# Kernel optimization log

Measured on AMD Instinct MI355X. Metric: run time of the kernel, lower is better.

## Reference

```python
import jax, jax.numpy as jnp
import numpy as np

EPS = 1e-5
K = 3
N_TAP = K * K


def _bn(x, g, b, m, v):
    # eval-mode batchnorm over channel axis 1 of NCHW
    inv = g / jnp.sqrt(v + EPS)
    return x * inv[None, :, None, None] + (b - m * inv)[None, :, None, None]


def _silu(x):
    return x * jax.nn.sigmoid(x)


def _dcn(x, offset, mask, w, b, pad=1):
    """Modulated deformable conv (DCNv2), stride 1.
    x: [B,C,H,W], offset: [B,2n,H,W] ((dy,dx) per tap), mask: [B,n,H,W],
    w: [O,C,K,K], b: [O]."""
    B, C, H, W = x.shape
    O = w.shape[0]
    ky, kx = jnp.meshgrid(jnp.arange(K), jnp.arange(K), indexing='ij')
    ky = ky.reshape(N_TAP).astype(x.dtype)
    kx = kx.reshape(N_TAP).astype(x.dtype)
    off = offset.reshape(B, N_TAP, 2, H, W)
    base_y = jnp.arange(H, dtype=x.dtype)[None, None, :, None]
    base_x = jnp.arange(W, dtype=x.dtype)[None, None, None, :]
    # fractional sample positions [B,n,H,W]
    py = base_y - pad + ky[None, :, None, None] + off[:, :, 0]
    px = base_x - pad + kx[None, :, None, None] + off[:, :, 1]
    y0 = jnp.floor(py)
    x0 = jnp.floor(px)
    fy = py - y0
    fx = px - x0
    y0i = y0.astype(jnp.int32)
    x0i = x0.astype(jnp.int32)
    x_flat = x.reshape(B, C, 1, H * W)

    def corner(yi, xi, wgt):
        valid = (yi >= 0) & (yi < H) & (xi >= 0) & (xi < W)
        idx = (jnp.clip(yi, 0, H - 1) * W + jnp.clip(xi, 0, W - 1)).reshape(B, 1, N_TAP, H * W)
        v = jnp.take_along_axis(x_flat, idx, axis=-1)  # [B,C,n,HW]
        return v * (wgt * valid.astype(x.dtype)).reshape(B, 1, N_TAP, H * W)

    acc = corner(y0i, x0i, (1 - fy) * (1 - fx))
    acc = acc + corner(y0i, x0i + 1, (1 - fy) * fx)
    acc = acc + corner(y0i + 1, x0i, fy * (1 - fx))
    acc = acc + corner(y0i + 1, x0i + 1, fy * fx)
    val = acc.reshape(B, C, N_TAP, H, W) * mask[:, None]  # modulation
    out = jnp.einsum('bcnhw,ocn->bohw', val, w.reshape(O, C, N_TAP))
    return out + b[None, :, None, None]


def setup_inputs() -> dict:
    key = jax.random.key(0)
    ks = jax.random.split(key, 16)
    B, C1, H, W = 8, 256, 80, 80
    C2 = 256
    Ch = 128  # c_ = int(c2 * 0.5)
    d = {}
    d['x'] = jax.random.normal(ks[0], (B, C1, H, W), jnp.float32)
    # cv1: 1x1 conv (no bias) + BN
    d['cv1_w'] = jax.random.normal(ks[1], (Ch, C1), jnp.float32) * (1.0 / np.sqrt(C1))
    d['bn1_g'] = jax.random.uniform(ks[2], (Ch,), jnp.float32, 0.5, 1.5)
    d['bn1_b'] = jax.random.normal(ks[3], (Ch,), jnp.float32) * 0.1
    d['bn1_m'] = jax.random.normal(ks[4], (Ch,), jnp.float32) * 0.1
    d['bn1_v'] = jax.random.uniform(ks[5], (Ch,), jnp.float32, 0.5, 1.5)
    # offset/mask predictor 3x3 conv (small weights -> modest deformation)
    d['off_w'] = jax.random.normal(ks[6], (3 * N_TAP, Ch, K, K), jnp.float32) * 0.01
    d['off_b'] = jnp.zeros((3 * N_TAP,), jnp.float32)
    # dcn main weight/bias
    d['dcn_w'] = jax.random.normal(ks[7], (Ch, Ch, K, K), jnp.float32) * (1.0 / np.sqrt(Ch * N_TAP))
    d['dcn_b'] = jnp.zeros((Ch,), jnp.float32)
    d['bn2_g'] = jax.random.uniform(ks[8], (Ch,), jnp.float32, 0.5, 1.5)
    d['bn2_b'] = jax.random.normal(ks[9], (Ch,), jnp.float32) * 0.1
    d['bn2_m'] = jax.random.normal(ks[10], (Ch,), jnp.float32) * 0.1
    d['bn2_v'] = jax.random.uniform(ks[11], (Ch,), jnp.float32, 0.5, 1.5)
    # cv2: 1x1 conv (no bias) + BN
    d['cv2_w'] = jax.random.normal(ks[12], (C2, Ch), jnp.float32) * (1.0 / np.sqrt(Ch))
    d['bn3_g'] = jax.random.uniform(ks[13], (C2,), jnp.float32, 0.5, 1.5)
    d['bn3_b'] = jax.random.normal(ks[14], (C2,), jnp.float32) * 0.1
    d['bn3_m'] = jax.random.normal(ks[15], (C2,), jnp.float32) * 0.1
    d['bn3_v'] = jnp.ones((C2,), jnp.float32)
    return d


def reference(x, cv1_w, bn1_g, bn1_b, bn1_m, bn1_v,
              off_w, off_b, dcn_w, dcn_b, bn2_g, bn2_b, bn2_m, bn2_v,
              cv2_w, bn3_g, bn3_b, bn3_m, bn3_v):
    # cv1: 1x1 conv -> BN -> SiLU
    y = _silu(_bn(jnp.einsum('bchw,oc->bohw', x, cv1_w), bn1_g, bn1_b, bn1_m, bn1_v))
    # offset/mask predictor: 3x3 conv, pad 1
    raw = jax.lax.conv_general_dilated(
        y, off_w, window_strides=(1, 1), padding=((1, 1), (1, 1)),
        dimension_numbers=('NCHW', 'OIHW', 'NCHW')) + off_b[None, :, None, None]
    offset = raw[:, :2 * N_TAP]
    mask = jax.nn.sigmoid(raw[:, 2 * N_TAP:])
    # modulated deformable 3x3 conv -> BN -> SiLU
    y = _silu(_bn(_dcn(y, offset, mask, dcn_w, dcn_b), bn2_g, bn2_b, bn2_m, bn2_v))
    # cv2: 1x1 conv -> BN -> SiLU
    y = _silu(_bn(jnp.einsum('bchw,oc->bohw', y, cv2_w), bn3_g, bn3_b, bn3_m, bn3_v))
    return x + y  # shortcut (c1 == c2)
```

## Files before the change

### kernel.cpp

```cpp
#include <hip/hip_runtime.h>
#include <math.h>

#define HWSZ 6400
#define WIMG 80
#define HIMG 80
#define BEPS 1e-5f

typedef __attribute__((ext_vector_type(8))) short short8;
typedef __attribute__((ext_vector_type(4))) float f32x4;

__device__ __forceinline__ unsigned short f2b(float f) {
    unsigned u = __builtin_bit_cast(unsigned, f);
    u += 0x7fffu + ((u >> 16) & 1u);
    return (unsigned short)(u >> 16);
}
__device__ __forceinline__ float b2f(unsigned short h) {
    unsigned u = ((unsigned)h) << 16;
    return __builtin_bit_cast(float, u);
}
__device__ __forceinline__ float silu_f(float t) { return t / (1.f + __expf(-t)); }

#define BPOS(sub, nt, n16, q) (((((sub)*4 + (nt))*16 + (n16))*40) + (q)*8)

__global__ __launch_bounds__(256) void k_prep(
    const float* __restrict__ cv1w, const float* __restrict__ g1, const float* __restrict__ b1,
    const float* __restrict__ m1, const float* __restrict__ v1,
    const float* __restrict__ offw, const float* __restrict__ offb,
    const float* __restrict__ dcnw, const float* __restrict__ dcnb,
    const float* __restrict__ g2, const float* __restrict__ b2,
    const float* __restrict__ m2, const float* __restrict__ v2,
    const float* __restrict__ cv2w, const float* __restrict__ g3, const float* __restrict__ b3,
    const float* __restrict__ m3, const float* __restrict__ v3,
    unsigned short* __restrict__ apk1, unsigned short* __restrict__ apko,
    unsigned short* __restrict__ apkd, unsigned short* __restrict__ apk2,
    float* __restrict__ bias1, float* __restrict__ biaso,
    float* __restrict__ bias2, float* __restrict__ bias3)
{
    int idx = blockIdx.x * 256 + threadIdx.x;
    if (idx < 32768) {
        int j = idx & 7, L = (idx >> 3) & 63, ks = (idx >> 9) & 7, mt = idx >> 12;
        int o = mt * 16 + (L & 15), k = ks * 32 + (L >> 4) * 8 + j;
        float inv = g1[o] * rsqrtf(v1[o] + BEPS);
        apk1[idx] = f2b(cv1w[o * 256 + k] * inv);
    } else if (idx < 69632) {
        int t = idx - 32768;
        int j = t & 7, L = (t >> 3) & 63;
        int mt = t / 18432, rem = t % 18432, ks = rem >> 9;
        int o = mt * 16 + (L & 15);
        int kp = ks * 32 + (L >> 4) * 8 + j;
        int n = kp >> 7, c = kp & 127;
        float wv = (o < 27) ? offw[(size_t)(o * 128 + c) * 9 + n] : 0.f;
        apko[t] = f2b(wv);
    } else if (idx < 217088) {
        int t = idx - 69632;
        int j = t & 7, L = (t >> 3) & 63;
        int mt = t / 18432, rem = t % 18432, ks = rem >> 9;
        int o = mt * 16 + (L & 15);
        int kp = ks * 32 + (L >> 4) * 8 + j;
        int n = kp >> 7, c = kp & 127;
        float inv = g2[o] * rsqrtf(v2[o] + BEPS);
        apkd[t] = f2b(dcnw[(size_t)(o * 128 + c) * 9 + n] * inv);
    } else if (idx < 249856) {
        int t = idx - 217088;
        int j = t & 7, L = (t >> 3) & 63, ks = (t >> 9) & 3, mt = t >> 11;
        int o = mt * 16 + (L & 15), k = ks * 32 + (L >> 4) * 8 + j;
        float inv = g3[o] * rsqrtf(v3[o] + BEPS);
        apk2[t] = f2b(cv2w[o * 128 + k] * inv);
    } else if (idx < 250395) {
        int t = idx - 249856;
        if (t < 128) { float inv = g1[t] * rsqrtf(v1[t] + BEPS); bias1[t] = b1[t] - m1[t] * inv; }
        else if (t < 155) { biaso[t - 128] = offb[t - 128]; }
        else if (t < 283) { int o = t - 155; float inv = g2[o] * rsqrtf(v2[o] + BEPS);
                            bias2[o] = dcnb[o] * inv + b2[o] - m2[o] * inv; }
        else { int o = t - 283; float inv = g3[o] * rsqrtf(v3[o] + BEPS); bias3[o] = b3[o] - m3[o] * inv; }
    }
}

__global__ __launch_bounds__(256) void k_cv1(
    const float* __restrict__ x, const unsigned short* __restrict__ apk1,
    const float* __restrict__ bias1, unsigned short* __restrict__ y1t)
{
    __shared__ __align__(16) unsigned short sB[20480];
    int blk = blockIdx.x;
    int b = blk / 100, pt = blk % 100;
    int p0 = pt * 64;
    int tid = threadIdx.x;
    int lane = tid & 63;
    int w = tid >> 6;
    {
        int px = lane, q = w;
        const float* xb = x + (size_t)b * 256 * HWSZ + p0 + px;
        for (int ks = 0; ks < 8; ++ks) {
            short8 v;
#pragma unroll
            for (int j = 0; j < 8; ++j)
                v[j] = (short)f2b(xb[(size_t)(ks * 32 + q * 8 + j) * HWSZ]);
            *(short8*)&sB[((ks * 4 + (px >> 4)) * 16 + (px & 15)) * 40 + q * 8] = v;
        }
    }
    __syncthreads();
    int n16 = lane & 15, qd = lane >> 4;
    f32x4 acc[2][4];
#pragma unroll
    for (int mi = 0; mi < 2; ++mi)
#pragma unroll
        for (int nt = 0; nt < 4; ++nt) acc[mi][nt] = (f32x4){0.f, 0.f, 0.f, 0.f};
    for (int ks = 0; ks < 8; ++ks) {
        short8 bf[4];
#pragma unroll
        for (int nt = 0; nt < 4; ++nt)
            bf[nt] = *(const short8*)&sB[((ks * 4 + nt) * 16 + n16) * 40 + qd * 8];
#pragma unroll
        for (int mi = 0; mi < 2; ++mi) {
            int mt = w * 2 + mi;
            short8 af = *(const short8*)&apk1[(size_t)((mt * 8 + ks) * 64 + lane) * 8];
#pragma unroll
            for (int nt = 0; nt < 4; ++nt)
                acc[mi][nt] = __builtin_amdgcn_mfma_f32_16x16x32_bf16(af, bf[nt], acc[mi][nt], 0, 0, 0);
        }
    }
    __syncthreads();
#pragma unroll
    for (int mi = 0; mi < 2; ++mi)
#pragma unroll
        for (int nt = 0; nt < 4; ++nt)
#pragma unroll
            for (int r = 0; r < 4; ++r) {
                int o = w * 32 + mi * 16 + qd * 4 + r;
                float sv = silu_f(acc[mi][nt][r] + bias1[o]);
                sB[(nt * 16 + n16) * 136 + o] = f2b(sv);
            }
    __syncthreads();
    {
        int px = tid >> 2, qq = tid & 3;
        unsigned short* ytb = y1t + ((size_t)b * HWSZ + p0 + px) * 128;
#pragma unroll
        for (int seg = 0; seg < 4; ++seg) {
            short8 v = *(const short8*)&sB[px * 136 + qq * 32 + seg * 8];
            *(short8*)&ytb[qq * 32 + seg * 8] = v;
        }
    }
}

__global__ __launch_bounds__(256) void k_off(
    const unsigned short* __restrict__ y1t, const unsigned short* __restrict__ apko,
    const float* __restrict__ biaso, float* __restrict__ raw)
{
    __shared__ __align__(16) unsigned short sV[10240];
    int blk = blockIdx.x;
    int b = blk / 100, pt = blk % 100;
    int p0 = pt * 64;
    int tid = threadIdx.x;
    int lane = tid & 63, w = tid >> 6;
    int n16 = lane & 15, qd = lane >> 4;
    int pxl = tid >> 2, q = tid & 3;
    int p = p0 + pxl;
    int h = p / WIMG, wx = p % WIMG;
    const unsigned short* yb = y1t + (size_t)b * HWSZ * 128;
    f32x4 acc[2];
    acc[0] = (f32x4){0.f, 0.f, 0.f, 0.f};
    acc[1] = (f32x4){0.f, 0.f, 0.f, 0.f};
    const short8 zz = {0, 0, 0, 0, 0, 0, 0, 0};
    for (int n = 0; n < 9; ++n) {
        int hh = h - 1 + n / 3, ww = wx - 1 + n % 3;
        bool valid = ((unsigned)hh < HIMG) && ((unsigned)ww < WIMG);
        int spx = valid ? hh * WIMG + ww : 0;
        const unsigned short* ys = yb + (size_t)spx * 128 + q * 8;
#pragma unroll
        for (int sub = 0; sub < 4; ++sub) {
            short8 v = *(const short8*)&ys[sub * 32];
            if (!valid) v = zz;
            *(short8*)&sV[BPOS(sub, pxl >> 4, pxl & 15, q)] = v;
        }
        __syncthreads();
#pragma unroll
        for (int sub = 0; sub < 4; ++sub) {
            int ks = n * 4 + sub;
            short8 bf = *(const short8*)&sV[BPOS(sub, w, n16, qd)];
#pragma unroll
            for (int mi = 0; mi < 2; ++mi) {
                short8 af = *(const short8*)&apko[(size_t)((mi * 36 + ks) * 64 + lane) * 8];
                acc[mi] = __builtin_amdgcn_mfma_f32_16x16x32_bf16(af, bf, acc[mi], 0, 0, 0);
            }
        }
        __syncthreads();
    }
    float* rb = raw + (size_t)b * 27 * HWSZ + p0 + w * 16 + n16;
#pragma unroll
    for (int mi = 0; mi < 2; ++mi)
#pragma unroll
        for (int r = 0; r < 4; ++r) {
            int o = mi * 16 + qd * 4 + r;
            if (o < 27) {
                float t = acc[mi][r] + biaso[o];
                if (o >= 18) t = 1.f / (1.f + __expf(-t));
                rb[(size_t)o * HWSZ] = t;
            }
        }
}

__global__ __launch_bounds__(256) void k_dcn(
    const unsigned short* __restrict__ y1t, const float* __restrict__ raw,
    const unsigned short* __restrict__ apkd, const float* __restrict__ bias2,
    unsigned short* __restrict__ zt)
{
    __shared__ float swgt[4][9][64];
    __shared__ unsigned short sidx[4][9][64];
    __shared__ __align__(16) unsigned short sV[10240];
    int blk = blockIdx.x;
    int b = blk / 100, pt = blk % 100;
    int p0 = pt * 64;
    int tid = threadIdx.x;

    for (int i = tid; i < 576; i += 256) {
        int n = i / 64, pp = i % 64;
        int p = p0 + pp;
        int h = p / WIMG, wx = p % WIMG;
        const float* rb = raw + (size_t)b * 27 * HWSZ + p;
        float dy = rb[(size_t)(2 * n) * HWSZ];
        float dx = rb[(size_t)(2 * n + 1) * HWSZ];
        float mk = rb[(size_t)(18 + n) * HWSZ];
        float py = (float)(h - 1 + n / 3) + dy;
        float px = (float)(wx - 1 + n % 3) + dx;
        float y0f = floorf(py), x0f = floorf(px);
        float fy = py - y0f, fx = px - x0f;
        int y0 = (int)y0f, x0 = (int)x0f;
#pragma unroll
        for (int k = 0; k < 4; ++k) {
            int yy = y0 + (k >> 1);
            int xx = x0 + (k & 1);
            bool valid = ((unsigned)yy < HIMG) && ((unsigned)xx < WIMG);
            float wk = ((k >> 1) ? fy : 1.f - fy) * ((k & 1) ? fx : 1.f - fx);
            wk = valid ? wk * mk : 0.f;
            int yc = min(max(yy, 0), HIMG - 1);
            int xc = min(max(xx, 0), WIMG - 1);
            sidx[k][n][pp] = (unsigned short)(yc * WIMG + xc);
            swgt[k][n][pp] = wk;
        }
    }
    __syncthreads();

    int lane = tid & 63, w = tid >> 6;
    int n16 = lane & 15, qd = lane >> 4;
    int pxl = tid >> 2, q = tid & 3;
    const unsigned short* yb = y1t + (size_t)b * HWSZ * 128;
    f32x4 acc[2][4];
#pragma unroll
    for (int mi = 0; mi < 2; ++mi)
#pragma unroll
        for (int nt = 0; nt < 4; ++nt) acc[mi][nt] = (f32x4){0.f, 0.f, 0.f, 0.f};

    for (int n = 0; n < 9; ++n) {
        float av[4][8];
#pragma unroll
        for (int sub = 0; sub < 4; ++sub)
#pragma unroll
            for (int j = 0; j < 8; ++j) av[sub][j] = 0.f;
#pragma unroll
        for (int k = 0; k < 4; ++k) {
            float wk = swgt[k][n][pxl];
            const unsigned short* ys = yb + (size_t)sidx[k][n][pxl] * 128 + q * 8;
#pragma unroll
            for (int sub = 0; sub < 4; ++sub) {
                short8 v = *(const short8*)&ys[sub * 32];
#pragma unroll
                for (int j = 0; j < 8; ++j)
                    av[sub][j] = fmaf(wk, b2f((unsigned short)v[j]), av[sub][j]);
            }
        }
#pragma unroll
        for (int sub = 0; sub < 4; ++sub) {
            short8 v;
#pragma unroll
            for (int j = 0; j < 8; ++j) v[j] = (short)f2b(av[sub][j]);
            *(short8*)&sV[BPOS(sub, pxl >> 4, pxl & 15, q)] = v;
        }
        __syncthreads();
#pragma unroll
        for (int sub = 0; sub < 4; ++sub) {
            int ks = n * 4 + sub;
            short8 bf[4];
#pragma unroll
            for (int nt = 0; nt < 4; ++nt)
                bf[nt] = *(const short8*)&sV[BPOS(sub, nt, n16, qd)];
#pragma unroll
            for (int mi = 0; mi < 2; ++mi) {
                short8 af = *(const short8*)&apkd[(size_t)(((2 * w + mi) * 36 + ks) * 64 + lane) * 8];
#pragma unroll
                for (int nt = 0; nt < 4; ++nt)
                    acc[mi][nt] = __builtin_amdgcn_mfma_f32_16x16x32_bf16(af, bf[nt], acc[mi][nt], 0, 0, 0);
            }
        }
        __syncthreads();
    }
#pragma unroll
    for (int mi = 0; mi < 2; ++mi)
#pragma unroll
        for (int nt = 0; nt < 4; ++nt)
#pragma unroll
            for (int r = 0; r < 4; ++r) {
                int o = w * 32 + mi * 16 + qd * 4 + r;
                float sv = silu_f(acc[mi][nt][r] + bias2[o]);
                sV[(nt * 16 + n16) * 136 + o] = f2b(sv);
            }
    __syncthreads();
    {
        int px = tid >> 2, qq = tid & 3;
        unsigned short* zb = zt + ((size_t)b * HWSZ + p0 + px) * 128;
#pragma unroll
        for (int seg = 0; seg < 4; ++seg) {
            short8 v = *(const short8*)&sV[px * 136 + qq * 32 + seg * 8];
            *(short8*)&zb[qq * 32 + seg * 8] = v;
        }
    }
}

__global__ __launch_bounds__(256) void k_cv2(
    const unsigned short* __restrict__ zt, const float* __restrict__ x,
    const unsigned short* __restrict__ apk2, const float* __restrict__ bias3,
    float* __restrict__ out)
{
    int blk = blockIdx.x;
    int b = blk / 100, pt = blk % 100;
    int p0 = pt * 64;
    int tid = threadIdx.x;
    int lane = tid & 63, w = tid >> 6;
    int n16 = lane & 15, qd = lane >> 4;
    const unsigned short* zb = zt + ((size_t)b * HWSZ + p0) * 128;
    f32x4 acc[4][4];
#pragma unroll
    for (int mi = 0; mi < 4; ++mi)
#pragma unroll
        for (int nt = 0; nt < 4; ++nt) acc[mi][nt] = (f32x4){0.f, 0.f, 0.f, 0.f};
#pragma unroll
    for (int ks = 0; ks < 4; ++ks) {
        short8 bf[4];
#pragma unroll
        for (int nt = 0; nt < 4; ++nt)
            bf[nt] = *(const short8*)&zb[(size_t)(nt * 16 + n16) * 128 + ks * 32 + qd * 8];
#pragma unroll
        for (int mi = 0; mi < 4; ++mi) {
            int mt = w * 4 + mi;
            short8 af = *(const short8*)&apk2[(size_t)((mt * 4 + ks) * 64 + lane) * 8];
#pragma unroll
            for (int nt = 0; nt < 4; ++nt)
                acc[mi][nt] = __builtin_amdgcn_mfma_f32_16x16x32_bf16(af, bf[nt], acc[mi][nt], 0, 0, 0);
        }
    }
    const float* xb = x + (size_t)b * 256 * HWSZ;
    float* ob = out + (size_t)b * 256 * HWSZ;
#pragma unroll
    for (int mi = 0; mi < 4; ++mi)
#pragma unroll
        for (int nt = 0; nt < 4; ++nt)
#pragma unroll
            for (int r = 0; r < 4; ++r) {
                int o = w * 64 + mi * 16 + qd * 4 + r;
                size_t idx = (size_t)o * HWSZ + p0 + nt * 16 + n16;
                ob[idx] = xb[idx] + silu_f(acc[mi][nt][r] + bias3[o]);
            }
}

extern "C" void kernel_launch(void* const* d_in, const int* in_sizes, int n_in,
                              void* d_out, int out_size, void* d_ws, size_t ws_size,
                              hipStream_t stream) {
    const float* x     = (const float*)d_in[0];
    const float* cv1w  = (const float*)d_in[1];
    const float* bn1g  = (const float*)d_in[2];
    const float* bn1b  = (const float*)d_in[3];
    const float* bn1m  = (const float*)d_in[4];
    const float* bn1v  = (const float*)d_in[5];
    const float* offw  = (const float*)d_in[6];
    const float* offb  = (const float*)d_in[7];
    const float* dcnw  = (const float*)d_in[8];
    const float* dcnb  = (const float*)d_in[9];
    const float* bn2g  = (const float*)d_in[10];
    const float* bn2b  = (const float*)d_in[11];
    const float* bn2m  = (const float*)d_in[12];
    const float* bn2v  = (const float*)d_in[13];
    const float* cv2w  = (const float*)d_in[14];
    const float* bn3g  = (const float*)d_in[15];
    const float* bn3b  = (const float*)d_in[16];
    const float* bn3m  = (const float*)d_in[17];
    const float* bn3v  = (const float*)d_in[18];
    float* out = (float*)d_out;

    float* base = (float*)d_ws;
    unsigned short* y1t = (unsigned short*)base;
    float* raw   = base + 3276800;
    unsigned short* zt  = (unsigned short*)(base + 4659200);
    unsigned short* apk1 = (unsigned short*)(base + 7936000);
    unsigned short* apko = (unsigned short*)(base + 7952384);
    unsigned short* apkd = (unsigned short*)(base + 7970816);
    unsigned short* apk2 = (unsigned short*)(base + 8044544);
    float* bias1 = base + 8060928;
    float* biaso = base + 8061056;
    float* bias2 = base + 8061088;
    float* bias3 = base + 8061216;

    k_prep<<<979, 256, 0, stream>>>(cv1w, bn1g, bn1b, bn1m, bn1v,
                                    offw, offb, dcnw, dcnb,
                                    bn2g, bn2b, bn2m, bn2v,
                                    cv2w, bn3g, bn3b, bn3m, bn3v,
                                    apk1, apko, apkd, apk2,
                                    bias1, biaso, bias2, bias3);
    k_cv1<<<800, 256, 0, stream>>>(x, apk1, bias1, y1t);
    k_off<<<800, 256, 0, stream>>>(y1t, apko, biaso, raw);
    k_dcn<<<800, 256, 0, stream>>>(y1t, raw, apkd, bias2, zt);
    k_cv2<<<800, 256, 0, stream>>>(zt, x, apk2, bias3, out);
}
```

Before: 235.9 us.

## Stage halo tiles in LDS for offset conv and deformable sampling, remap blocks

Measured after the change: 262.8 us. 11.4% more time.

```diff
diff --git a/kernel.cpp b/kernel.cpp
--- a/kernel.cpp
+++ b/kernel.cpp
@@ -8,6 +8,7 @@
 
 typedef __attribute__((ext_vector_type(8))) short short8;
 typedef __attribute__((ext_vector_type(4))) float f32x4;
+typedef __attribute__((ext_vector_type(4))) unsigned u32x4;
 
 __device__ __forceinline__ unsigned short f2b(float f) {
     unsigned u = __builtin_bit_cast(unsigned, f);
@@ -20,7 +21,7 @@
 }
 __device__ __forceinline__ float silu_f(float t) { return t / (1.f + __expf(-t)); }
 
-#define BPOS(sub, nt, n16, q) (((((sub)*4 + (nt))*16 + (n16))*40) + (q)*8)
+__device__ __forceinline__ int remap800(int blk) { return (blk & 7) * 100 + (blk >> 3); }
 
 __global__ __launch_bounds__(256) void k_prep(
     const float* __restrict__ cv1w, const float* __restrict__ g1, const float* __restrict__ b1,
@@ -81,7 +82,7 @@
     const float* __restrict__ bias1, unsigned short* __restrict__ y1t)
 {
     __shared__ __align__(16) unsigned short sB[20480];
-    int blk = blockIdx.x;
+    int blk = remap800(blockIdx.x);
     int b = blk / 100, pt = blk % 100;
     int p0 = pt * 64;
     int tid = threadIdx.x;
@@ -146,44 +147,48 @@
     const unsigned short* __restrict__ y1t, const unsigned short* __restrict__ apko,
     const float* __restrict__ biaso, float* __restrict__ raw)
 {
-    __shared__ __align__(16) unsigned short sV[10240];
-    int blk = blockIdx.x;
+    __shared__ __align__(16) unsigned short sV[227 * 136];
+    int blk = remap800(blockIdx.x);
     int b = blk / 100, pt = blk % 100;
     int p0 = pt * 64;
     int tid = threadIdx.x;
+    const unsigned short* yb = y1t + (size_t)b * HWSZ * 128;
+    for (int c = tid; c < 226 * 16; c += 256) {
+        int row = c >> 4, col = c & 15;
+        int sp = p0 - 81 + row;
+        sp = min(max(sp, 0), HWSZ - 1);
+        *(short8*)&sV[row * 136 + col * 8] = *(const short8*)&yb[(size_t)sp * 128 + col * 8];
+    }
+    if (tid < 16) {
+        short8 z = {0, 0, 0, 0, 0, 0, 0, 0};
+        *(short8*)&sV[226 * 136 + tid * 8] = z;
+    }
+    __syncthreads();
+
     int lane = tid & 63, w = tid >> 6;
     int n16 = lane & 15, qd = lane >> 4;
-    int pxl = tid >> 2, q = tid & 3;
-    int p = p0 + pxl;
+    int p = p0 + w * 16 + n16;
     int h = p / WIMG, wx = p % WIMG;
-    const unsigned short* yb = y1t + (size_t)b * HWSZ * 128;
     f32x4 acc[2];
     acc[0] = (f32x4){0.f, 0.f, 0.f, 0.f};
     acc[1] = (f32x4){0.f, 0.f, 0.f, 0.f};
-    const short8 zz = {0, 0, 0, 0, 0, 0, 0, 0};
+#pragma unroll
     for (int n = 0; n < 9; ++n) {
-        int hh = h - 1 + n / 3, ww = wx - 1 + n % 3;
+        int dh = n / 3 - 1, dw = n % 3 - 1;
+        int hh = h + dh, ww = wx + dw;
         bool valid = ((unsigned)hh < HIMG) && ((unsigned)ww < WIMG);
-        int spx = valid ? hh * WIMG + ww : 0;
-        const unsigned short* ys = yb + (size_t)spx * 128 + q * 8;
-#pragma unroll
-        for (int sub = 0; sub < 4; ++sub) {
-            short8 v = *(const short8*)&ys[sub * 32];
-            if (!valid) v = zz;
-            *(short8*)&sV[BPOS(sub, pxl >> 4, pxl & 15, q)] = v;
-        }
-        __syncthreads();
-#pragma unroll
-        for (int sub = 0; sub < 4; ++sub) {
-            int ks = n * 4 + sub;
-            short8 bf = *(const short8*)&sV[BPOS(sub, w, n16, qd)];
+        int row = valid ? (81 + w * 16 + n16 + dh * WIMG + dw) : 226;
+        const unsigned short* rV = &sV[row * 136 + qd * 8];
+#pragma unroll
+        for (int s = 0; s < 4; ++s) {
+            int ks = n * 4 + s;
+            short8 bf = *(const short8*)&rV[s * 32];
 #pragma unroll
             for (int mi = 0; mi < 2; ++mi) {
                 short8 af = *(const short8*)&apko[(size_t)((mi * 36 + ks) * 64 + lane) * 8];
                 acc[mi] = __builtin_amdgcn_mfma_f32_16x16x32_bf16(af, bf, acc[mi], 0, 0, 0);
             }
         }
-        __syncthreads();
     }
     float* rb = raw + (size_t)b * 27 * HWSZ + p0 + w * 16 + n16;
 #pragma unroll
@@ -199,23 +204,50 @@
         }
 }
 
-__global__ __launch_bounds__(256) void k_dcn(
+#define HY 12
+#define HX 12
+#define NHALO 144
+
+#define ACC8(uu, cb)                                                                   \
+    {                                                                                  \
+        _Pragma("unroll") for (int t = 0; t < 4; ++t) {                                \
+            unsigned uv = (uu)[t];                                                     \
+            av[(cb) + 2 * t] = fmaf(wk, __builtin_bit_cast(float, uv << 16),           \
+                                    av[(cb) + 2 * t]);                                 \
+            av[(cb) + 2 * t + 1] = fmaf(wk, __builtin_bit_cast(float, uv & 0xffff0000u),\
+                                        av[(cb) + 2 * t + 1]);                         \
+        }                                                                              \
+    }
+
+__global__ __launch_bounds__(256, 2) void k_dcn(
     const unsigned short* __restrict__ y1t, const float* __restrict__ raw,
     const unsigned short* __restrict__ apkd, const float* __restrict__ bias2,
     unsigned short* __restrict__ zt)
 {
-    __shared__ float swgt[4][9][64];
+    __shared__ __align__(16) unsigned short sH[NHALO * 128];
+    __shared__ __align__(16) unsigned short sB[64 * 136];
+    __shared__ float swy[2][9][64];
+    __shared__ unsigned short sfx[9][64];
     __shared__ unsigned short sidx[4][9][64];
-    __shared__ __align__(16) unsigned short sV[10240];
-    int blk = blockIdx.x;
+
+    int blk = remap800(blockIdx.x);
     int b = blk / 100, pt = blk % 100;
-    int p0 = pt * 64;
+    int h0 = (pt / 10) * 8, w0 = (pt % 10) * 8;
     int tid = threadIdx.x;
-
+    const unsigned short* yb = y1t + (size_t)b * HWSZ * 128;
+
+    for (int i = tid; i < NHALO * 16; i += 256) {
+        int r = i >> 4, u = i & 15;
+        int ly = r / HX, lx = r % HX;
+        int yy = min(max(h0 + ly - 2, 0), HIMG - 1);
+        int xx = min(max(w0 + lx - 2, 0), WIMG - 1);
+        *(u32x4*)&sH[r * 128 + (u ^ (r & 7)) * 8] =
+            *(const u32x4*)&yb[(size_t)(yy * WIMG + xx) * 128 + u * 8];
+    }
     for (int i = tid; i < 576; i += 256) {
-        int n = i / 64, pp = i % 64;
-        int p = p0 + pp;
-        int h = p / WIMG, wx = p % WIMG;
+        int n = i / 64, pp = i & 63;
+        int h = h0 + (pp >> 3), wx = w0 + (pp & 7);
+        int p = h * WIMG + wx;
         const float* rb = raw + (size_t)b * 27 * HWSZ + p;
         float dy = rb[(size_t)(2 * n) * HWSZ];
         float dx = rb[(size_t)(2 * n + 1) * HWSZ];
@@ -225,17 +257,17 @@
         float y0f = floorf(py), x0f = floorf(px);
         float fy = py - y0f, fx = px - x0f;
         int y0 = (int)y0f, x0 = (int)x0f;
+        swy[0][n][pp] = (1.f - fy) * mk;
+        swy[1][n][pp] = fy * mk;
+        sfx[n][pp] = __builtin_bit_cast(unsigned short, (_Float16)fx);
 #pragma unroll
         for (int k = 0; k < 4; ++k) {
             int yy = y0 + (k >> 1);
             int xx = x0 + (k & 1);
-            bool valid = ((unsigned)yy < HIMG) && ((unsigned)xx < WIMG);
-            float wk = ((k >> 1) ? fy : 1.f - fy) * ((k & 1) ? fx : 1.f - fx);
-            wk = valid ? wk * mk : 0.f;
+            unsigned valid = (((unsigned)yy < HIMG) && ((unsigned)xx < WIMG)) ? 0x8000u : 0u;
             int yc = min(max(yy, 0), HIMG - 1);
             int xc = min(max(xx, 0), WIMG - 1);
-            sidx[k][n][pp] = (unsigned short)(yc * WIMG + xc);
-            swgt[k][n][pp] = wk;
+            sidx[k][n][pp] = (unsigned short)((yc << 7) | xc | valid);
         }
     }
     __syncthreads();
@@ -243,7 +275,6 @@
     int lane = tid & 63, w = tid >> 6;
     int n16 = lane & 15, qd = lane >> 4;
     int pxl = tid >> 2, q = tid & 3;
-    const unsigned short* yb = y1t + (size_t)b * HWSZ * 128;
     f32x4 acc[2][4];
 #pragma unroll
     for (int mi = 0; mi < 2; ++mi)
@@ -251,29 +282,47 @@
         for (int nt = 0; nt < 4; ++nt) acc[mi][nt] = (f32x4){0.f, 0.f, 0.f, 0.f};
 
     for (int n = 0; n < 9; ++n) {
-        float av[4][8];
-#pragma unroll
-        for (int sub = 0; sub < 4; ++sub)
-#pragma unroll
-            for (int j = 0; j < 8; ++j) av[sub][j] = 0.f;
+        float av[32];
+#pragma unroll
+        for (int j = 0; j < 32; ++j) av[j] = 0.f;
+        float fxv = (float)__builtin_bit_cast(_Float16, sfx[n][pxl]);
+        float fx1 = 1.f - fxv;
+        float wy0 = swy[0][n][pxl], wy1 = swy[1][n][pxl];
 #pragma unroll
         for (int k = 0; k < 4; ++k) {
-            float wk = swgt[k][n][pxl];
-            const unsigned short* ys = yb + (size_t)sidx[k][n][pxl] * 128 + q * 8;
-#pragma unroll
-            for (int sub = 0; sub < 4; ++sub) {
-                short8 v = *(const short8*)&ys[sub * 32];
-#pragma unroll
-                for (int j = 0; j < 8; ++j)
-                    av[sub][j] = fmaf(wk, b2f((unsigned short)v[j]), av[sub][j]);
-            }
-        }
-#pragma unroll
-        for (int sub = 0; sub < 4; ++sub) {
-            short8 v;
-#pragma unroll
-            for (int j = 0; j < 8; ++j) v[j] = (short)f2b(av[sub][j]);
-            *(short8*)&sV[BPOS(sub, pxl >> 4, pxl & 15, q)] = v;
+            unsigned s = sidx[k][n][pxl];
+            float wk = ((k >> 1) ? wy1 : wy0) * ((k & 1) ? fxv : fx1);
+            if (!(s & 0x8000u)) wk = 0.f;
+            int yc = (int)((s >> 7) & 127u), xc = (int)(s & 127u);
+            int ly = yc - h0 + 2, lx = xc - w0 + 2;
+            if (((unsigned)ly < HY) && ((unsigned)lx < HX)) {
+                int r = ly * HX + lx;
+                const unsigned short* hb = &sH[r * 128];
+                int xr = r & 7;
+                u32x4 u0 = *(const u32x4*)&hb[((q * 4 + 0) ^ xr) * 8];
+                u32x4 u1 = *(const u32x4*)&hb[((q * 4 + 1) ^ xr) * 8];
+                u32x4 u2 = *(const u32x4*)&hb[((q * 4 + 2) ^ xr) * 8];
+                u32x4 u3 = *(const u32x4*)&hb[((q * 4 + 3) ^ xr) * 8];
+                ACC8(u0, 0) ACC8(u1, 8) ACC8(u2, 16) ACC8(u3, 24)
+            } else if (wk != 0.f) {
+                const unsigned short* src = &yb[(size_t)(yc * WIMG + xc) * 128 + q * 32];
+                u32x4 u0 = *(const u32x4*)src;
+                u32x4 u1 = *(const u32x4*)(src + 8);
+                u32x4 u2 = *(const u32x4*)(src + 16);
+                u32x4 u3 = *(const u32x4*)(src + 24);
+                ACC8(u0, 0) ACC8(u1, 8) ACC8(u2, 16) ACC8(u3, 24)
+            }
+        }
+        unsigned pk[16];
+#pragma unroll
+        for (int t = 0; t < 16; ++t)
+            asm("v_cvt_pk_bf16_f32 %0, %1, %2" : "=v"(pk[t]) : "v"(av[2 * t]), "v"(av[2 * t + 1]));
+        {
+            unsigned short* dst = &sB[pxl * 136 + q * 32];
+            *(u32x4*)dst        = (u32x4){pk[0], pk[1], pk[2], pk[3]};
+            *(u32x4*)(dst + 8)  = (u32x4){pk[4], pk[5], pk[6], pk[7]};
+            *(u32x4*)(dst + 16) = (u32x4){pk[8], pk[9], pk[10], pk[11]};
+            *(u32x4*)(dst + 24) = (u32x4){pk[12], pk[13], pk[14], pk[15]};
         }
         __syncthreads();
 #pragma unroll
@@ -282,7 +331,7 @@
             short8 bf[4];
 #pragma unroll
             for (int nt = 0; nt < 4; ++nt)
-                bf[nt] = *(const short8*)&sV[BPOS(sub, nt, n16, qd)];
+                bf[nt] = *(const short8*)&sB[(nt * 16 + n16) * 136 + sub * 32 + qd * 8];
 #pragma unroll
             for (int mi = 0; mi < 2; ++mi) {
                 short8 af = *(const short8*)&apkd[(size_t)(((2 * w + mi) * 36 + ks) * 64 + lane) * 8];
@@ -301,15 +350,16 @@
             for (int r = 0; r < 4; ++r) {
                 int o = w * 32 + mi * 16 + qd * 4 + r;
                 float sv = silu_f(acc[mi][nt][r] + bias2[o]);
-                sV[(nt * 16 + n16) * 136 + o] = f2b(sv);
+                sB[(nt * 16 + n16) * 136 + o] = f2b(sv);
             }
     __syncthreads();
     {
         int px = tid >> 2, qq = tid & 3;
-        unsigned short* zb = zt + ((size_t)b * HWSZ + p0 + px) * 128;
+        int p = (h0 + (px >> 3)) * WIMG + w0 + (px & 7);
+        unsigned short* zb = zt + ((size_t)b * HWSZ + p) * 128;
 #pragma unroll
         for (int seg = 0; seg < 4; ++seg) {
-            short8 v = *(const short8*)&sV[px * 136 + qq * 32 + seg * 8];
+            short8 v = *(const short8*)&sB[px * 136 + qq * 32 + seg * 8];
             *(short8*)&zb[qq * 32 + seg * 8] = v;
         }
     }
@@ -320,7 +370,7 @@
     const unsigned short* __restrict__ apk2, const float* __restrict__ bias3,
     float* __restrict__ out)
 {
-    int blk = blockIdx.x;
+    int blk = remap800(blockIdx.x);
     int b = blk / 100, pt = blk % 100;
     int p0 = pt * 64;
     int tid = threadIdx.x;
```
